# Kernel tuning notes

Measured on AMD Instinct MI355X. Metric: run time of the kernel, lower is better.

Reference implementation:

```python
import jax, jax.numpy as jnp
import numpy as np

# Circuit structure constants (match init_kwargs)
N_NODES = 32768        # number of sum nodes in this layer
N_CHILD = 65536        # number of child nodes
NNZ = 1048576          # number of sparse weight entries (avg fan-in 32)
BATCH = 128


def setup_inputs() -> dict:
    key = jax.random.key(0)
    k1, k2, k3, k4 = jax.random.split(key, 4)
    # child log-likelihoods per sample (output of child layers)
    child_ll = jax.random.normal(k1, (BATCH, N_CHILD), dtype=jnp.float32)
    # sparse log-weights of the BCOO weight matrix [N_NODES, N_CHILD]
    log_w = jax.random.normal(k2, (NNZ,), dtype=jnp.float32)
    rows = jnp.sort(jax.random.randint(k3, (NNZ,), 0, N_NODES)).astype(jnp.int64)
    cols = jax.random.randint(k4, (NNZ,), 0, N_CHILD).astype(jnp.int64)
    return {"child_ll": child_ll, "log_w": log_w, "rows": rows, "cols": cols}


def reference(child_ll, log_w, rows, cols):
    """Faithful jax translation of SumLayer.log_likelihood_of_nodes.

    Original: per sample, exponentiate BCOO log-weights and child
    log-likelihoods, sparse matvec (weights @ exp(child_ll)), then
    log(result) - log_normalization_constants, where the normalization
    constants are log(row-sums of exp(log_weights)).
    """
    w = jnp.exp(log_w)  # [NNZ]
    # log normalization constants: log of row-sums of exp(log_weights)
    log_z = jnp.log(jax.ops.segment_sum(w, rows, num_segments=N_NODES))  # [N_NODES]

    def per_sample(ll):  # ll: [N_CHILD]
        p = jnp.exp(ll)
        contrib = w * p[cols]                                   # gather + weight [NNZ]
        return jax.ops.segment_sum(contrib, rows, num_segments=N_NODES)  # [N_NODES]

    s = jax.vmap(per_sample)(child_ll)  # [BATCH, N_NODES]
    return jnp.log(s) - log_z
```

## Files before the change

### kernel.cpp

```cpp
#include <hip/hip_runtime.h>
#include <hip/hip_fp16.h>
#include <math.h>

#define BATCH     128
#define N_NODES   32768
#define N_CHILD   65536
#define NNZ_TOTAL 1048576

__global__ __launch_bounds__(256) void exp_transpose_kernel(
    const float* __restrict__ child_ll, __half* __restrict__ ex) {
    __shared__ float tile[64][BATCH + 1];
    const int c0 = blockIdx.x * 64;
    const int t  = threadIdx.x;

    {
        const int cl = t & 63;
        const int b0 = t >> 6;
#pragma unroll
        for (int j = 0; j < BATCH / 4; ++j) {
            const int b = b0 + j * 4;
            tile[cl][b] = expf(child_ll[(size_t)b * N_CHILD + c0 + cl]);
        }
    }
    __syncthreads();

    {
        const int cl = t >> 4;
        const int b0 = (t & 15) * 8;
#pragma unroll
        for (int p = 0; p < 4; ++p) {
            const int c = p * 16 + cl;
            union { __half2 h[4]; uint4 u; } pk;
#pragma unroll
            for (int k = 0; k < 4; ++k)
                pk.h[k] = __half2{__float2half(tile[c][b0 + 2 * k]),
                                  __float2half(tile[c][b0 + 2 * k + 1])};
            *(uint4*)&ex[(size_t)(c0 + c) * BATCH + b0] = pk.u;
        }
    }
}

__global__ __launch_bounds__(256) void exp_w_kernel(
    const float* __restrict__ log_w, float* __restrict__ w) {
    const int i = (blockIdx.x * 256 + threadIdx.x) * 4;
    float4 v = *(const float4*)&log_w[i];
    v.x = expf(v.x); v.y = expf(v.y); v.z = expf(v.z); v.w = expf(v.w);
    *(float4*)&w[i] = v;
}

__global__ __launch_bounds__(256) void row_starts_kernel(
    const int* __restrict__ rows, int* __restrict__ row_start) {
    const int r = blockIdx.x * blockDim.x + threadIdx.x;
    if (r > N_NODES) return;
    if (r == N_NODES) { row_start[r] = NNZ_TOTAL; return; }
    int lo = 0, hi = NNZ_TOTAL;
    while (lo < hi) {
        const int mid = (lo + hi) >> 1;
        if (rows[mid] < r) lo = mid + 1; else hi = mid;
    }
    row_start[r] = lo;
}

__global__ __launch_bounds__(256, 4) void sum_rows_kernel(
    const __half* __restrict__ ex, const float* __restrict__ w,
    const int* __restrict__ cols, const int* __restrict__ row_start,
    float* __restrict__ out) {
    const int wave = threadIdx.x >> 6;
    const int lane = threadIdx.x & 63;
    const int bid  = blockIdx.x;
    const int rb   = (bid & 7) * (N_NODES / 4 / 8) + (bid >> 3);
    const int r    = rb * 4 + wave;

    const int start = row_start[r];
    const int end   = row_start[r + 1];
    const char* exb = (const char*)ex;
    const unsigned bo = ((unsigned)lane & 15u) * 16u;
    const int pbase = (lane >> 4) * 4;

    float acc[8] = {0.f, 0.f, 0.f, 0.f, 0.f, 0.f, 0.f, 0.f};
    float wlane = 0.f;

    for (int base = start; base < end; base += 64) {
        const int  idx   = base + lane;
        const bool valid = idx < end;
        const int   c  = __builtin_nontemporal_load(&cols[valid ? idx : start]);
        const float wv = valid ? __builtin_nontemporal_load(&w[idx]) : 0.f;
        wlane += wv;
        const int seg = end - base;

#pragma unroll
        for (int h = 0; h < 2; ++h) {
            const int hb = h * 32;
            if (hb >= seg) break;

            int  ct[8];
            float wt[8];
            uint4 g[8];

#pragma unroll
            for (int q = 0; q < 4; ++q) {
                if (hb + q * 8 < seg) {
#pragma unroll
                    for (int u = 0; u < 2; ++u) {
                        const int t = q * 2 + u;
                        const int pa = pbase + (hb + 4 * t) * 4;
                        ct[t] = __builtin_amdgcn_ds_bpermute(pa, c);
                        wt[t] = __uint_as_float(__builtin_amdgcn_ds_bpermute(
                            pa, __float_as_uint(wv)));
                    }
                }
            }
#pragma unroll
            for (int q = 0; q < 4; ++q) {
                if (hb + q * 8 < seg) {
#pragma unroll
                    for (int u = 0; u < 2; ++u) {
                        const int t = q * 2 + u;
                        g[t] = *(const uint4*)(exb +
                                ((size_t)(unsigned)ct[t] << 8) + bo);
                    }
                }
            }
#pragma unroll
            for (int q = 0; q < 4; ++q) {
                if (hb + q * 8 < seg) {
#pragma unroll
                    for (int u = 0; u < 2; ++u) {
                        const int t = q * 2 + u;
                        const __half2* hp = (const __half2*)&g[t];
#pragma unroll
                        for (int k = 0; k < 4; ++k) {
                            const float2 f = __half22float2(hp[k]);
                            acc[2 * k]     = fmaf(wt[t], f.x, acc[2 * k]);
                            acc[2 * k + 1] = fmaf(wt[t], f.y, acc[2 * k + 1]);
                        }
                    }
                }
            }
        }
    }

#pragma unroll
    for (int k = 0; k < 8; ++k) {
        acc[k] += __shfl_xor(acc[k], 16, 64);
        acc[k] += __shfl_xor(acc[k], 32, 64);
    }
    float wsum = wlane;
#pragma unroll
    for (int m = 1; m < 64; m <<= 1) wsum += __shfl_xor(wsum, m, 64);
    const float logz = logf(wsum);

    if (lane < 16) {
        const int b0 = lane * 8;
#pragma unroll
        for (int k = 0; k < 8; ++k)
            out[(size_t)(b0 + k) * N_NODES + r] = logf(acc[k]) - logz;
    }
}

extern "C" void kernel_launch(void* const* d_in, const int* in_sizes, int n_in,
                              void* d_out, int out_size, void* d_ws, size_t ws_size,
                              hipStream_t stream) {
    const float* child_ll = (const float*)d_in[0];
    const float* log_w    = (const float*)d_in[1];
    const int*   rows     = (const int*)d_in[2];
    const int*   cols     = (const int*)d_in[3];
    float*       out      = (float*)d_out;

    __half* ex        = (__half*)d_ws;
    float*  w         = (float*)((char*)d_ws + (size_t)N_CHILD * BATCH * 2);
    int*    row_start = (int*)((char*)w + (size_t)NNZ_TOTAL * 4);

    exp_transpose_kernel<<<N_CHILD / 64, 256, 0, stream>>>(child_ll, ex);
    exp_w_kernel<<<NNZ_TOTAL / 1024, 256, 0, stream>>>(log_w, w);
    row_starts_kernel<<<(N_NODES + 256) / 256 + 1, 256, 0, stream>>>(rows, row_start);
    sum_rows_kernel<<<N_NODES / 4, 256, 0, stream>>>(ex, w, cols, row_start, out);
}
```

Baseline: 69.04 us.

## Split batch into quarters per XCD pair to shrink per-XCD gather working set

The sum-rows kernel now launches four times as many blocks, and each wave handles one batch quarter (32 samples, 64 bytes) of its row instead of all 128 samples. XCD pairs (derived from the block index) are mapped to the same batch quarter, so each XCD's L2 only caches a quarter of the transposed fp16 exp table. Each lane group now covers 16 nonzeros per step with 4-lane sub-slots, and the reduction adds two more shuffle stages. The cost is that cols, w and row_start are read four times and every row's nonzero loop is repeated per quarter.

Measured after the change: 103.2 us. +49.5%, slower.

```diff
diff --git a/kernel.cpp b/kernel.cpp
--- a/kernel.cpp
+++ b/kernel.cpp
@@ -68,14 +68,18 @@
     const int wave = threadIdx.x >> 6;
     const int lane = threadIdx.x & 63;
     const int bid  = blockIdx.x;
-    const int rb   = (bid & 7) * (N_NODES / 4 / 8) + (bid >> 3);
-    const int r    = rb * 4 + wave;
+    const int xcd  = bid & 7;
+    const int quarter = xcd >> 1;
+    const int parity  = xcd & 1;
+    const int rowblk  = (bid >> 3) * 2 + parity;
+    const int r       = rowblk * 4 + wave;
 
     const int start = row_start[r];
     const int end   = row_start[r + 1];
     const char* exb = (const char*)ex;
-    const unsigned bo = ((unsigned)lane & 15u) * 16u;
-    const int pbase = (lane >> 4) * 4;
+    const int  gslot = lane >> 2;
+    const unsigned sub = (unsigned)lane & 3u;
+    const unsigned qoff = (unsigned)quarter * 64u + sub * 16u;
 
     float acc[8] = {0.f, 0.f, 0.f, 0.f, 0.f, 0.f, 0.f, 0.f};
     float wlane = 0.f;
@@ -88,53 +92,33 @@
         wlane += wv;
         const int seg = end - base;
 
-#pragma unroll
-        for (int h = 0; h < 2; ++h) {
-            const int hb = h * 32;
-            if (hb >= seg) break;
-
-            int  ct[8];
-            float wt[8];
-            uint4 g[8];
+        int   ct[4];
+        float wt[4];
+        uint4 g[4];
 
 #pragma unroll
-            for (int q = 0; q < 4; ++q) {
-                if (hb + q * 8 < seg) {
+        for (int t = 0; t < 4; ++t) {
+            if (t * 16 < seg) {
+                const int pa = (t * 16 + gslot) * 4;
+                ct[t] = __builtin_amdgcn_ds_bpermute(pa, c);
+                wt[t] = __uint_as_float(__builtin_amdgcn_ds_bpermute(
+                    pa, __float_as_uint(wv)));
+            }
+        }
 #pragma unroll
-                    for (int u = 0; u < 2; ++u) {
-                        const int t = q * 2 + u;
-                        const int pa = pbase + (hb + 4 * t) * 4;
-                        ct[t] = __builtin_amdgcn_ds_bpermute(pa, c);
-                        wt[t] = __uint_as_float(__builtin_amdgcn_ds_bpermute(
-                            pa, __float_as_uint(wv)));
-                    }
-                }
-            }
+        for (int t = 0; t < 4; ++t) {
+            if (t * 16 < seg)
+                g[t] = *(const uint4*)(exb + ((size_t)(unsigned)ct[t] << 8) + qoff);
+        }
 #pragma unroll
-            for (int q = 0; q < 4; ++q) {
-                if (hb + q * 8 < seg) {
+        for (int t = 0; t < 4; ++t) {
+            if (t * 16 < seg) {
+                const __half2* hp = (const __half2*)&g[t];
 #pragma unroll
-                    for (int u = 0; u < 2; ++u) {
-                        const int t = q * 2 + u;
-                        g[t] = *(const uint4*)(exb +
-                                ((size_t)(unsigned)ct[t] << 8) + bo);
-                    }
-                }
-            }
-#pragma unroll
-            for (int q = 0; q < 4; ++q) {
-                if (hb + q * 8 < seg) {
-#pragma unroll
-                    for (int u = 0; u < 2; ++u) {
-                        const int t = q * 2 + u;
-                        const __half2* hp = (const __half2*)&g[t];
-#pragma unroll
-                        for (int k = 0; k < 4; ++k) {
-                            const float2 f = __half22float2(hp[k]);
-                            acc[2 * k]     = fmaf(wt[t], f.x, acc[2 * k]);
-                            acc[2 * k + 1] = fmaf(wt[t], f.y, acc[2 * k + 1]);
-                        }
-                    }
+                for (int k = 0; k < 4; ++k) {
+                    const float2 f = __half22float2(hp[k]);
+                    acc[2 * k]     = fmaf(wt[t], f.x, acc[2 * k]);
+                    acc[2 * k + 1] = fmaf(wt[t], f.y, acc[2 * k + 1]);
                 }
             }
         }
@@ -142,6 +126,8 @@
 
 #pragma unroll
     for (int k = 0; k < 8; ++k) {
+        acc[k] += __shfl_xor(acc[k], 4, 64);
+        acc[k] += __shfl_xor(acc[k], 8, 64);
         acc[k] += __shfl_xor(acc[k], 16, 64);
         acc[k] += __shfl_xor(acc[k], 32, 64);
     }
@@ -150,8 +136,8 @@
     for (int m = 1; m < 64; m <<= 1) wsum += __shfl_xor(wsum, m, 64);
     const float logz = logf(wsum);
 
-    if (lane < 16) {
-        const int b0 = lane * 8;
+    if (lane < 4) {
+        const int b0 = quarter * 32 + (int)sub * 8;
 #pragma unroll
         for (int k = 0; k < 8; ++k)
             out[(size_t)(b0 + k) * N_NODES + r] = logf(acc[k]) - logz;
@@ -174,5 +160,5 @@
     exp_transpose_kernel<<<N_CHILD / 64, 256, 0, stream>>>(child_ll, ex);
     exp_w_kernel<<<NNZ_TOTAL / 1024, 256, 0, stream>>>(log_w, w);
     row_starts_kernel<<<(N_NODES + 256) / 256 + 1, 256, 0, stream>>>(rows, row_start);
-    sum_rows_kernel<<<N_NODES / 4, 256, 0, stream>>>(ex, w, cols, row_start, out);
+    sum_rows_kernel<<<N_NODES / 4 * 4, 256, 0, stream>>>(ex, w, cols, row_start, out);
 }
```

## Store exp(child_ll) as per-child-scaled FP8 and fold scale into weights

Applied to the files above, without the earlier changes.

Exponentiated child log-likelihoods are now stored as FP8 with a power-of-two scale per child, chosen from that child's maximum over the batch. The inverse scale is folded into precomputed per-edge weights, so the gather reads 128 bytes per child instead of 256 and halves the dominant random-gather traffic. The weight-exp and row-start kernels are merged into one launch. The normalizer is recomputed from log_w inside the main kernel. The risk is accuracy: FP8 has few mantissa bits, and small values underflow relative to the per-child max, which may exceed the tolerance.

Measured after the change: 70.88 us. +2.7%, slower.

```diff
diff --git a/kernel.cpp b/kernel.cpp
--- a/kernel.cpp
+++ b/kernel.cpp
@@ -1,5 +1,4 @@
 #include <hip/hip_runtime.h>
-#include <hip/hip_fp16.h>
 #include <math.h>
 
 #define BATCH     128
@@ -7,9 +6,13 @@
 #define N_CHILD   65536
 #define NNZ_TOTAL 1048576
 
-__global__ __launch_bounds__(256) void exp_transpose_kernel(
-    const float* __restrict__ child_ll, __half* __restrict__ ex) {
+typedef __attribute__((ext_vector_type(2))) float fx2;
+
+__global__ __launch_bounds__(256) void exp_transpose_fp8_kernel(
+    const float* __restrict__ child_ll, unsigned char* __restrict__ ex8,
+    float* __restrict__ winv) {
     __shared__ float tile[64][BATCH + 1];
+    __shared__ float sc[64];
     const int c0 = blockIdx.x * 64;
     const int t  = threadIdx.x;
 
@@ -24,47 +27,72 @@
     }
     __syncthreads();
 
+    if (t < 64) {
+        float m = tile[t][0];
+#pragma unroll 4
+        for (int b = 1; b < BATCH; ++b) m = fmaxf(m, tile[t][b]);
+        const int k = 7 - ilogbf(m);
+        sc[t] = ldexpf(1.f, k);
+        winv[c0 + t] = ldexpf(1.f, -k);
+    }
+    __syncthreads();
+
     {
-        const int cl = t >> 4;
-        const int b0 = (t & 15) * 8;
+        const int sub = t & 7;
+        const int b0  = sub * 16;
 #pragma unroll
-        for (int p = 0; p < 4; ++p) {
-            const int c = p * 16 + cl;
-            union { __half2 h[4]; uint4 u; } pk;
+        for (int p = 0; p < 2; ++p) {
+            const int c = (t >> 3) + p * 32;
+            const float s = sc[c];
+            uint4 o;
+            unsigned* ow = (unsigned*)&o;
 #pragma unroll
-            for (int k = 0; k < 4; ++k)
-                pk.h[k] = __half2{__float2half(tile[c][b0 + 2 * k]),
-                                  __float2half(tile[c][b0 + 2 * k + 1])};
-            *(uint4*)&ex[(size_t)(c0 + c) * BATCH + b0] = pk.u;
+            for (int q = 0; q < 4; ++q) {
+                unsigned v = 0;
+                v = __builtin_amdgcn_cvt_pk_fp8_f32(
+                        tile[c][b0 + q * 4 + 0] * s, tile[c][b0 + q * 4 + 1] * s, v, false);
+                v = __builtin_amdgcn_cvt_pk_fp8_f32(
+                        tile[c][b0 + q * 4 + 2] * s, tile[c][b0 + q * 4 + 3] * s, v, true);
+                ow[q] = v;
+            }
+            *(uint4*)&ex8[(size_t)(c0 + c) * 128 + (unsigned)b0] = o;
         }
     }
 }
 
-__global__ __launch_bounds__(256) void exp_w_kernel(
-    const float* __restrict__ log_w, float* __restrict__ w) {
-    const int i = (blockIdx.x * 256 + threadIdx.x) * 4;
-    float4 v = *(const float4*)&log_w[i];
-    v.x = expf(v.x); v.y = expf(v.y); v.z = expf(v.z); v.w = expf(v.w);
-    *(float4*)&w[i] = v;
-}
-
-__global__ __launch_bounds__(256) void row_starts_kernel(
-    const int* __restrict__ rows, int* __restrict__ row_start) {
-    const int r = blockIdx.x * blockDim.x + threadIdx.x;
-    if (r > N_NODES) return;
-    if (r == N_NODES) { row_start[r] = NNZ_TOTAL; return; }
-    int lo = 0, hi = NNZ_TOTAL;
-    while (lo < hi) {
-        const int mid = (lo + hi) >> 1;
-        if (rows[mid] < r) lo = mid + 1; else hi = mid;
+__global__ __launch_bounds__(256) void prep_kernel(
+    const float* __restrict__ log_w, const int* __restrict__ cols,
+    const float* __restrict__ winv, const int* __restrict__ rows,
+    float* __restrict__ wfold, int* __restrict__ row_start) {
+    const int bid = blockIdx.x;
+    const int t   = threadIdx.x;
+    if (bid < 1024) {
+        const int i = (bid * 256 + t) * 4;
+        const float4 lw = *(const float4*)&log_w[i];
+        const int4   cc = *(const int4*)&cols[i];
+        float4 o;
+        o.x = expf(lw.x) * winv[cc.x];
+        o.y = expf(lw.y) * winv[cc.y];
+        o.z = expf(lw.z) * winv[cc.z];
+        o.w = expf(lw.w) * winv[cc.w];
+        *(float4*)&wfold[i] = o;
+    } else {
+        const int r = (bid - 1024) * 256 + t;
+        if (r > N_NODES) return;
+        if (r == N_NODES) { row_start[r] = NNZ_TOTAL; return; }
+        int lo = 0, hi = NNZ_TOTAL;
+        while (lo < hi) {
+            const int mid = (lo + hi) >> 1;
+            if (rows[mid] < r) lo = mid + 1; else hi = mid;
+        }
+        row_start[r] = lo;
     }
-    row_start[r] = lo;
 }
 
 __global__ __launch_bounds__(256, 4) void sum_rows_kernel(
-    const __half* __restrict__ ex, const float* __restrict__ w,
-    const int* __restrict__ cols, const int* __restrict__ row_start,
-    float* __restrict__ out) {
+    const unsigned char* __restrict__ ex8, const float* __restrict__ wfold,
+    const float* __restrict__ log_w, const int* __restrict__ cols,
+    const int* __restrict__ row_start, float* __restrict__ out) {
     const int wave = threadIdx.x >> 6;
     const int lane = threadIdx.x & 63;
     const int bid  = blockIdx.x;
@@ -73,75 +101,63 @@
 
     const int start = row_start[r];
     const int end   = row_start[r + 1];
-    const char* exb = (const char*)ex;
-    const unsigned bo = ((unsigned)lane & 15u) * 16u;
-    const int pbase = (lane >> 4) * 4;
+    const int  slot = lane >> 3;
+    const unsigned sub = (unsigned)lane & 7u;
+    const unsigned boff = sub * 16u;
 
-    float acc[8] = {0.f, 0.f, 0.f, 0.f, 0.f, 0.f, 0.f, 0.f};
+    float acc[16];
+#pragma unroll
+    for (int k = 0; k < 16; ++k) acc[k] = 0.f;
     float wlane = 0.f;
 
     for (int base = start; base < end; base += 64) {
         const int  idx   = base + lane;
         const bool valid = idx < end;
         const int   c  = __builtin_nontemporal_load(&cols[valid ? idx : start]);
-        const float wv = valid ? __builtin_nontemporal_load(&w[idx]) : 0.f;
-        wlane += wv;
+        const float wf = valid ? __builtin_nontemporal_load(&wfold[idx]) : 0.f;
+        wlane += valid ? expf(__builtin_nontemporal_load(&log_w[idx])) : 0.f;
         const int seg = end - base;
 
-#pragma unroll
-        for (int h = 0; h < 2; ++h) {
-            const int hb = h * 32;
-            if (hb >= seg) break;
-
-            int  ct[8];
-            float wt[8];
-            uint4 g[8];
+        int   ct[8];
+        float wt[8];
+        uint4 g[8];
 
 #pragma unroll
-            for (int q = 0; q < 4; ++q) {
-                if (hb + q * 8 < seg) {
+        for (int t8 = 0; t8 < 8; ++t8) {
+            if (t8 * 8 < seg) {
+                const int pa = (t8 * 8 + slot) * 4;
+                ct[t8] = __builtin_amdgcn_ds_bpermute(pa, c);
+                wt[t8] = __uint_as_float(__builtin_amdgcn_ds_bpermute(
+                    pa, __float_as_uint(wf)));
+            }
+        }
 #pragma unroll
-                    for (int u = 0; u < 2; ++u) {
-                        const int t = q * 2 + u;
-                        const int pa = pbase + (hb + 4 * t) * 4;
-                        ct[t] = __builtin_amdgcn_ds_bpermute(pa, c);
-                        wt[t] = __uint_as_float(__builtin_amdgcn_ds_bpermute(
-                            pa, __float_as_uint(wv)));
-                    }
-                }
-            }
+        for (int t8 = 0; t8 < 8; ++t8) {
+            if (t8 * 8 < seg)
+                g[t8] = *(const uint4*)(ex8 +
+                        ((size_t)(unsigned)ct[t8] << 7) + boff);
+        }
 #pragma unroll
-            for (int q = 0; q < 4; ++q) {
-                if (hb + q * 8 < seg) {
+        for (int t8 = 0; t8 < 8; ++t8) {
+            if (t8 * 8 < seg) {
+                const float wtv = wt[t8];
+                const unsigned* gu = (const unsigned*)&g[t8];
 #pragma unroll
-                    for (int u = 0; u < 2; ++u) {
-                        const int t = q * 2 + u;
-                        g[t] = *(const uint4*)(exb +
-                                ((size_t)(unsigned)ct[t] << 8) + bo);
-                    }
-                }
-            }
-#pragma unroll
-            for (int q = 0; q < 4; ++q) {
-                if (hb + q * 8 < seg) {
-#pragma unroll
-                    for (int u = 0; u < 2; ++u) {
-                        const int t = q * 2 + u;
-                        const __half2* hp = (const __half2*)&g[t];
-#pragma unroll
-                        for (int k = 0; k < 4; ++k) {
-                            const float2 f = __half22float2(hp[k]);
-                            acc[2 * k]     = fmaf(wt[t], f.x, acc[2 * k]);
-                            acc[2 * k + 1] = fmaf(wt[t], f.y, acc[2 * k + 1]);
-                        }
-                    }
+                for (int q = 0; q < 4; ++q) {
+                    const fx2 lo = __builtin_amdgcn_cvt_pk_f32_fp8((int)gu[q], false);
+                    const fx2 hi = __builtin_amdgcn_cvt_pk_f32_fp8((int)gu[q], true);
+                    acc[q * 4 + 0] = fmaf(wtv, lo.x, acc[q * 4 + 0]);
+                    acc[q * 4 + 1] = fmaf(wtv, lo.y, acc[q * 4 + 1]);
+                    acc[q * 4 + 2] = fmaf(wtv, hi.x, acc[q * 4 + 2]);
+                    acc[q * 4 + 3] = fmaf(wtv, hi.y, acc[q * 4 + 3]);
                 }
             }
         }
     }
 
 #pragma unroll
-    for (int k = 0; k < 8; ++k) {
+    for (int k = 0; k < 16; ++k) {
+        acc[k] += __shfl_xor(acc[k], 8, 64);
         acc[k] += __shfl_xor(acc[k], 16, 64);
         acc[k] += __shfl_xor(acc[k], 32, 64);
     }
@@ -150,10 +166,10 @@
     for (int m = 1; m < 64; m <<= 1) wsum += __shfl_xor(wsum, m, 64);
     const float logz = logf(wsum);
 
-    if (lane < 16) {
-        const int b0 = lane * 8;
+    if (lane < 8) {
+        const int b0 = lane * 16;
 #pragma unroll
-        for (int k = 0; k < 8; ++k)
+        for (int k = 0; k < 16; ++k)
             out[(size_t)(b0 + k) * N_NODES + r] = logf(acc[k]) - logz;
     }
 }
@@ -167,12 +183,14 @@
     const int*   cols     = (const int*)d_in[3];
     float*       out      = (float*)d_out;
 
-    __half* ex        = (__half*)d_ws;
-    float*  w         = (float*)((char*)d_ws + (size_t)N_CHILD * BATCH * 2);
-    int*    row_start = (int*)((char*)w + (size_t)NNZ_TOTAL * 4);
+    unsigned char* ex8    = (unsigned char*)d_ws;
+    float* winv      = (float*)((char*)d_ws + (size_t)N_CHILD * 128);
+    float* wfold     = (float*)((char*)winv + (size_t)N_CHILD * 4);
+    int*   row_start = (int*)((char*)wfold + (size_t)NNZ_TOTAL * 4);
 
-    exp_transpose_kernel<<<N_CHILD / 64, 256, 0, stream>>>(child_ll, ex);
-    exp_w_kernel<<<NNZ_TOTAL / 1024, 256, 0, stream>>>(log_w, w);
-    row_starts_kernel<<<(N_NODES + 256) / 256 + 1, 256, 0, stream>>>(rows, row_start);
-    sum_rows_kernel<<<N_NODES / 4, 256, 0, stream>>>(ex, w, cols, row_start, out);
+    exp_transpose_fp8_kernel<<<N_CHILD / 64, 256, 0, stream>>>(child_ll, ex8, winv);
+    prep_kernel<<<1024 + 129, 256, 0, stream>>>(log_w, cols, winv, rows,
+                                                wfold, row_start);
+    sum_rows_kernel<<<N_NODES / 4, 256, 0, stream>>>(ex8, wfold, log_w, cols,
+                                                     row_start, out);
 }
```
